# Performance work log

Hardware: AMD Instinct MI355X
Metric: run time of the kernel (lower is better)

Reference implementation:

```python
import jax, jax.numpy as jnp
import numpy as np

N = 96            # max_nodes == R (all nodes real)
IN_DIM, HID, ZD = 64, 256, 64
E = 1024
U = N * (N - 1) // 2
NUM_LOGITS = U + N   # 4656
MPM_ITERS = 50
BN_EPS = 1e-5

def _xavier_relu(k, fi, fo):
    # xavier_uniform with gain('relu') = sqrt(2)
    s = (2.0 ** 0.5) * (6.0 / (fi + fo)) ** 0.5
    return jax.random.uniform(k, (fi, fo), jnp.float32, -s, s)

def setup_inputs() -> dict:
    key = jax.random.key(0)
    ks = jax.random.split(key, 12)
    x = jax.random.normal(ks[0], (N, IN_DIM), jnp.float32)
    edge_index = jnp.stack([jax.random.randint(ks[1], (E,), 0, N),
                            jax.random.randint(ks[2], (E,), 0, N)]).astype(jnp.int32)
    a = (jax.random.uniform(ks[3], (N, N)) < 0.06).astype(jnp.float32)
    adj_gt = jnp.maximum(a, a.T) * (1.0 - jnp.eye(N, dtype=jnp.float32))
    return dict(
        x=x, edge_index=edge_index, adj_gt=adj_gt,
        W1=_xavier_relu(ks[4], IN_DIM, HID), b1=jnp.zeros(HID, jnp.float32),
        gamma1=jnp.ones(HID, jnp.float32), beta1=jnp.zeros(HID, jnp.float32),
        W2=_xavier_relu(ks[5], HID, HID), b2=jnp.zeros(HID, jnp.float32),
        gamma2=jnp.ones(HID, jnp.float32), beta2=jnp.zeros(HID, jnp.float32),
        Wmu=_xavier_relu(ks[6], HID, ZD), bmu=jnp.zeros(ZD, jnp.float32),
        Wlv=_xavier_relu(ks[7], HID, ZD), blv=jnp.zeros(ZD, jnp.float32),
        Wd1=_xavier_relu(ks[8], ZD, HID), bd1=jnp.zeros(HID, jnp.float32),
        Wd2=_xavier_relu(ks[9], HID, NUM_LOGITS), bd2=jnp.zeros(NUM_LOGITS, jnp.float32),
        eps=jax.random.normal(ks[10], (ZD,), jnp.float32))

def _bn(h, g, b):
    # BatchNorm1d, training mode: normalize over nodes (axis 0)
    m = h.mean(0)
    v = h.var(0)
    return (h - m) * jax.lax.rsqrt(v + BN_EPS) * g + b

def _forward(x, adj_gt, W1, b1, gamma1, beta1, W2, b2, gamma2, beta2,
             Wmu, bmu, Wlv, blv, Wd1, bd1, Wd2, bd2, eps, edge_index):
    ar = jnp.arange(N)
    eye = jnp.eye(N, dtype=bool)
    A = jnp.zeros((N, N), jnp.float32).at[edge_index[0], edge_index[1]].set(1.0)
    A = jnp.maximum(A, jnp.eye(N, dtype=jnp.float32))  # self loops
    dinv = jax.lax.rsqrt(A.sum(1))
    A_norm = A * dinv[:, None] * dinv[None, :]
    h = jax.nn.relu(_bn(A_norm @ (x @ W1) + b1, gamma1, beta1))
    h = jax.nn.relu(_bn(A_norm @ (h @ W2) + b2, gamma2, beta2))
    # ---- readout, reparam, decode ----
    g_vec = h.sum(0) / N                      # divide by real node count R
    mu = g_vec @ Wmu + bmu
    lv = jnp.clip(g_vec @ Wlv + blv, -4.0, 4.0)
    z = mu + eps * jnp.exp(0.5 * lv)
    vec = jnp.tanh(jax.nn.relu(z @ Wd1 + bd1) @ Wd2 + bd2)  # [NUM_LOGITS]
    # ---- vec_to_adj ----
    iu = jnp.triu_indices(N, 1)
    Ah = jnp.zeros((N, N), jnp.float32).at[iu].set(vec[:U])
    Ah = (Ah + Ah.T).at[ar, ar].set(vec[U:])  # adjacency logits
    # ---- edge similarity tensor S[i,j,a,b] ----
    Agt = adj_gt.at[ar, ar].set(1.0)
    B = jax.nn.sigmoid(Ah).at[ar, ar].set(1.0)
    degA, degB = Agt.sum(1), B.sum(1)
    node_sim = 1.0 / (jnp.abs(degA[:, None] - degB[None, :]) + 1.0)  # [N,N]
    dA, dB = jnp.diag(Agt), jnp.diag(B)
    S = (Agt[:, :, None, None] * dA[:, None, None, None] * dA[None, :, None, None]
         * B[None, None, :, :] * dB[None, None, :, None] * dB[None, None, None, :])
    xor = eye[:, :, None, None] ^ eye[None, None, :, :]
    S = jnp.where(xor, 0.0, S)
    diag_val = dA[:, None] * dB[None, :] * node_sim  # value at (i,i,a,a)
    both = eye[:, :, None, None] & eye[None, None, :, :]
    S = jnp.where(both, diag_val[:, None, :, None], S)
    # ---- MPM iteration (fixed 50 steps) ----
    nd = S[ar[:, None], ar[:, None], ar[None, :], ar[None, :]]  # node sim [N,N]
    offmask = (~eye)[:, :, None].astype(S.dtype)                # [N,N,1] over (i,j)
    def step(X, _):
        node_term = X * nd
        XS_max = (S * X[None, :, None, :]).max(-1)  # (i,j,a): max_b X[j,b]*S[i,j,a,b]
        edge_term = (XS_max * offmask).sum(1)       # sum over j != i
        Xn = node_term + edge_term
        Xn = Xn / jnp.linalg.norm(Xn)               # Frobenius norm
        return Xn, None
    X0 = jnp.full((N, N), 1.0 / N, jnp.float32)
    X, _ = jax.lax.scan(jax.checkpoint(step), X0, None, length=MPM_ITERS)
    return X

def reference(x, edge_index, adj_gt, W1, b1, gamma1, beta1, W2, b2, gamma2, beta2,
              Wmu, bmu, Wlv, blv, Wd1, bd1, Wd2, bd2, eps):
    return _forward(x, adj_gt, W1, b1, gamma1, beta1, W2, b2, gamma2, beta2,
                    Wmu, bmu, Wlv, blv, Wd1, bd1, Wd2, bd2, eps, edge_index)
```

## Files before the change

kernel.cpp:

```cpp
#include <hip/hip_runtime.h>
#include <math.h>

#define NN    96
#define EE    1024
#define HID   256
#define IND   64
#define ZD    64
#define NL    4656
#define NBLK  96
#define NTHR  384
#define ITERS 50
#define NBARS 57
#define SHF   (HID*49)

struct Params {
  const float* x; const int* ei; const float* adj;
  const float* W1; const float* b1; const float* g1; const float* be1;
  const float* W2; const float* b2; const float* g2; const float* be2;
  const float* Wmu; const float* bmu; const float* Wlv; const float* blv;
  const float* Wd1; const float* bd1; const float* Wd2; const float* bd2;
  const float* eps; float* out;
};

__device__ float d_XW[NN*HID];
__device__ float d_H1pre[NN*HID];
__device__ float d_HW2[NN*HID];
__device__ float d_H2pre[NN*HID];
__device__ float d_mean1[HID], d_istd1[HID];
__device__ float d_gvec[HID];
__device__ float d_vec[NL];
__device__ float d_Xg[2][NN*NN];
__device__ float d_ssq[ITERS+1];
__device__ int   d_flag[NBLK];
__device__ int   d_epoch;

__device__ __forceinline__ float gld(const float* p) {
  return __hip_atomic_load(p, __ATOMIC_RELAXED, __HIP_MEMORY_SCOPE_AGENT);
}
__device__ __forceinline__ void gst(float* p, float v) {
  __hip_atomic_store(p, v, __ATOMIC_RELAXED, __HIP_MEMORY_SCOPE_AGENT);
}

__device__ __forceinline__ float wsum(float v) {
  v += __shfl_xor(v, 32, 64);
  v += __shfl_xor(v, 16, 64);
  v += __shfl_xor(v,  8, 64);
  v += __shfl_xor(v,  4, 64);
  v += __shfl_xor(v,  2, 64);
  v += __shfl_xor(v,  1, 64);
  return v;
}

__device__ __forceinline__ int tri_idx(int a, int c) {
  return a*95 - (a*(a-1))/2 + (c - a - 1);
}

__device__ __forceinline__ void gbar(int idx, int base) {
  asm volatile("s_waitcnt vmcnt(0)" ::: "memory");
  __syncthreads();
  const int tgt = base + idx + 1;
  if (threadIdx.x == 0)
    __hip_atomic_store(&d_flag[blockIdx.x], tgt, __ATOMIC_RELAXED, __HIP_MEMORY_SCOPE_AGENT);
  if (threadIdx.x < NBLK) {
    while (__hip_atomic_load(&d_flag[threadIdx.x], __ATOMIC_RELAXED, __HIP_MEMORY_SCOPE_AGENT) < tgt)
      __builtin_amdgcn_s_sleep(2);
  }
  __syncthreads();
}

__global__ void __launch_bounds__(NTHR) gvae_kernel(Params p) {
  const int b = blockIdx.x;
  const int t = threadIdx.x;

  __shared__ __align__(16) float SH[SHF];
  __shared__ float pre1[HID];
  __shared__ float sg[HID], sd1[HID], sz[ZD];
  __shared__ float dinv[NN];
  __shared__ float eV[NN];   __shared__ int eL[NN];  __shared__ int s_ecnt;
  __shared__ float ndrow[NN], rowsq[NN];    __shared__ int nbrL[NN];
  __shared__ float sdegA;    __shared__ int s_cnt;

  const int base = __hip_atomic_load(&d_epoch, __ATOMIC_RELAXED, __HIP_MEMORY_SCOPE_AGENT) * NBARS;

  for (int i = t; i < NN*97; i += NTHR) SH[i] = 0.0f;
  __syncthreads();
  for (int e = t; e < EE; e += NTHR) {
    int s = p.ei[e], d = p.ei[EE + e];
    SH[s*97 + d] = 1.0f;
  }
  if (t < NN) SH[t*97 + t] = 1.0f;
  __syncthreads();
  if (t < NN) {
    float s = 0.0f;
    for (int j = 0; j < NN; ++j) s += SH[t*97 + j];
    dinv[t] = 1.0f / sqrtf(s);
  }
  if (t < 64) {
    bool is1 = SH[b*97 + t] > 0.5f;
    unsigned long long m1 = __ballot(is1);
    if (is1) eL[__popcll(m1 & ((1ull << t) - 1))] = t;
    int c1 = __popcll(m1);
    bool is2 = (t < 32) && SH[b*97 + 64 + t] > 0.5f;
    unsigned long long m2 = __ballot(is2);
    if (is2) eL[c1 + __popcll(m2 & ((1ull << t) - 1))] = 64 + t;
    if (t == 0) s_ecnt = c1 + __popcll(m2);
  }
  __syncthreads();
  if (t < s_ecnt) eV[t] = dinv[b] * dinv[eL[t]];
  if (t < HID) {
    float acc = 0.0f;
    for (int d = 0; d < IND; ++d) acc += p.x[b*IND + d] * p.W1[d*HID + t];
    gst(&d_XW[b*HID + t], acc);
  }
  if (t < NN) gst(&d_Xg[0][b*NN + t], 1.0f/96.0f);
  if (b == 0 && t <= ITERS) gst(&d_ssq[t], (t == 0) ? 1.0f : 0.0f);
  gbar(0, base);

  {
    const int lim = s_ecnt * HID;
    float tv[16];
    #pragma unroll
    for (int r = 0; r < 16; ++r) {
      int idx = t + r*NTHR;
      if (idx < lim) tv[r] = gld(&d_XW[eL[idx >> 8]*HID + (idx & 255)]);
    }
    #pragma unroll
    for (int r = 0; r < 16; ++r) {
      int idx = t + r*NTHR;
      if (idx < lim) SH[idx] = tv[r];
    }
    for (int idx = t + 16*NTHR; idx < lim; idx += NTHR)
      SH[idx] = gld(&d_XW[eL[idx >> 8]*HID + (idx & 255)]);
    __syncthreads();
    if (t < HID) {
      float acc = 0.0f;
      const int ec = s_ecnt;
      for (int n = 0; n < ec; ++n) acc += eV[n] * SH[n*HID + t];
      acc += p.b1[t];
      pre1[t] = acc;
      gst(&d_H1pre[b*HID + t], acc);
    }
  }
  gbar(1, base);

  if (b < 86) {
    int w = t >> 6, lane = t & 63;
    int c = b*3 + w;
    if (w < 3 && c < HID) {
      float v0 = gld(&d_H1pre[lane*HID + c]);
      float v1 = (lane < 32) ? gld(&d_H1pre[(64+lane)*HID + c]) : 0.0f;
      float mean = wsum(v0 + v1) * (1.0f/96.0f);
      float a0 = v0 - mean, a1 = (lane < 32) ? (v1 - mean) : 0.0f;
      float var = wsum(a0*a0 + a1*a1) * (1.0f/96.0f);
      if (lane == 0) { gst(&d_mean1[c], mean); gst(&d_istd1[c], 1.0f/sqrtf(var + 1e-5f)); }
    }
  }
  gbar(2, base);

  if (t < HID) {
    float m = gld(&d_mean1[t]), is = gld(&d_istd1[t]);
    pre1[t] = fmaxf((pre1[t] - m) * is * p.g1[t] + p.be1[t], 0.0f);
  }
  __syncthreads();
  if (t < HID) {
    float acc = 0.0f;
    for (int k = 0; k < HID; ++k) acc += pre1[k] * p.W2[k*HID + t];
    gst(&d_HW2[b*HID + t], acc);
  }
  gbar(3, base);

  {
    const int lim = s_ecnt * HID;
    float tv[16];
    #pragma unroll
    for (int r = 0; r < 16; ++r) {
      int idx = t + r*NTHR;
      if (idx < lim) tv[r] = gld(&d_HW2[eL[idx >> 8]*HID + (idx & 255)]);
    }
    #pragma unroll
    for (int r = 0; r < 16; ++r) {
      int idx = t + r*NTHR;
      if (idx < lim) SH[idx] = tv[r];
    }
    for (int idx = t + 16*NTHR; idx < lim; idx += NTHR)
      SH[idx] = gld(&d_HW2[eL[idx >> 8]*HID + (idx & 255)]);
    __syncthreads();
    if (t < HID) {
      float acc = 0.0f;
      const int ec = s_ecnt;
      for (int n = 0; n < ec; ++n) acc += eV[n] * SH[n*HID + t];
      acc += p.b2[t];
      gst(&d_H2pre[b*HID + t], acc);
    }
  }
  gbar(4, base);

  if (b < 86) {
    int w = t >> 6, lane = t & 63;
    int c = b*3 + w;
    if (w < 3 && c < HID) {
      float v0 = gld(&d_H2pre[lane*HID + c]);
      float v1 = (lane < 32) ? gld(&d_H2pre[(64+lane)*HID + c]) : 0.0f;
      float mean = wsum(v0 + v1) * (1.0f/96.0f);
      float a0 = v0 - mean, a1 = (lane < 32) ? (v1 - mean) : 0.0f;
      float var = wsum(a0*a0 + a1*a1) * (1.0f/96.0f);
      float is = 1.0f / sqrtf(var + 1e-5f);
      float ga = p.g2[c], be = p.be2[c];
      float h0 = fmaxf((v0 - mean)*is*ga + be, 0.0f);
      float h1v = (lane < 32) ? fmaxf((v1 - mean)*is*ga + be, 0.0f) : 0.0f;
      float gs = wsum(h0 + h1v);
      if (lane == 0) gst(&d_gvec[c], gs * (1.0f/96.0f));
    }
  }
  gbar(5, base);

  if (t < HID) sg[t] = gld(&d_gvec[t]);
  __syncthreads();
  if (t < ZD) {
    float am = p.bmu[t], al = p.blv[t];
    for (int c = 0; c < HID; ++c) {
      float gv = sg[c];
      am += gv * p.Wmu[c*ZD + t];
      al += gv * p.Wlv[c*ZD + t];
    }
    al = fminf(fmaxf(al, -4.0f), 4.0f);
    sz[t] = am + p.eps[t] * expf(0.5f * al);
  }
  __syncthreads();
  if (t < HID) {
    float acc = p.bd1[t];
    for (int d = 0; d < ZD; ++d) acc += sz[d] * p.Wd1[d*HID + t];
    sd1[t] = fmaxf(acc, 0.0f);
  }
  __syncthreads();
  {
    const int o0 = b*49;
    const int nout = min(49, NL - o0);
    #pragma unroll 4
    for (int idx = t; idx < HID*49; idx += NTHR) {
      int k = idx / 49, o = idx - k*49;
      SH[idx] = (o0 + o < NL) ? p.Wd2[k*NL + o0 + o] : 0.0f;
    }
    __syncthreads();
    if (t < nout) {
      float acc = p.bd2[o0 + t];
      for (int k = 0; k < HID; ++k) acc += sd1[k] * SH[k*49 + t];
      gst(&d_vec[o0 + t], tanhf(acc));
    }
  }
  gbar(6, base);

  {
    float tv[13];
    #pragma unroll
    for (int r = 0; r < 13; ++r) {
      int idx = t + r*NTHR;
      if (idx < NL) tv[r] = gld(&d_vec[idx]);
    }
    #pragma unroll
    for (int r = 0; r < 13; ++r) {
      int idx = t + r*NTHR;
      if (idx < NL) SH[idx] = tv[r];
    }
  }
  const int kk = t >> 2;
  const int qq = t & 3;
  if (t < 64) {
    float s = p.adj[b*NN + t] + ((t < 32) ? p.adj[b*NN + 64 + t] : 0.0f);
    s = wsum(s);
    if (t == 0) sdegA = s + 1.0f;
    bool is1 = (t != b) && (p.adj[b*NN + t] > 0.5f);
    unsigned long long m1 = __ballot(is1);
    if (is1) nbrL[__popcll(m1 & ((1ull << t) - 1))] = t;
    int c1 = __popcll(m1);
    bool is2 = (t < 32) && ((64 + t) != b) && (p.adj[b*NN + 64 + t] > 0.5f);
    unsigned long long m2 = __ballot(is2);
    if (is2) nbrL[c1 + __popcll(m2 & ((1ull << t) - 1))] = 64 + t;
    if (t == 0) s_cnt = c1 + __popcll(m2);
  }
  __syncthreads();

  float breg[24];
  {
    float bs = 0.0f;
    const int lb = qq*24;
    #pragma unroll
    for (int s = 0; s < 24; ++s) {
      int l = lb + s;
      float v = 0.0f;
      if (l != kk) {
        int a  = kk < l ? kk : l;
        int cc = kk < l ? l : kk;
        v = 1.0f / (1.0f + expf(-SH[tri_idx(a, cc)]));
      }
      breg[s] = v;
      bs += v;
    }
    float tot = bs + __shfl_xor(bs, 1, 64);
    tot += __shfl_xor(tot, 2, 64);
    if (qq == 0) ndrow[kk] = 1.0f / (fabsf(sdegA - (tot + 1.0f)) + 1.0f);
  }
  __syncthreads();

  int cur = 0;
  for (int it = 0; it < ITERS; ++it) {
    float s2 = gld(&d_ssq[it]);
    int ex;
    (void)frexpf(sqrtf(s2), &ex);
    float scale = ldexpf(1.0f, -ex);
    const int cnt = s_cnt;
    const int lim = (cnt + 1) * NN;
    const float* Xs = d_Xg[cur];
    {
      float tv[8];
      #pragma unroll
      for (int r = 0; r < 8; ++r) {
        int idx = t + r*NTHR;
        if (idx < lim) {
          int slot = idx / NN, col = idx - slot*NN;
          int j = (slot == cnt) ? b : nbrL[slot];
          tv[r] = gld(&Xs[j*NN + col]);
        }
      }
      #pragma unroll
      for (int r = 0; r < 8; ++r) {
        int idx = t + r*NTHR;
        if (idx < lim) SH[idx] = tv[r] * scale;
      }
      for (int idx = t + 8*NTHR; idx < lim; idx += NTHR) {
        int slot = idx / NN, col = idx - slot*NN;
        int j = (slot == cnt) ? b : nbrL[slot];
        SH[idx] = gld(&Xs[j*NN + col]) * scale;
      }
    }
    __syncthreads();

    float acc = 0.0f;
    for (int n = 0; n < cnt; ++n) {
      const float4* xp = reinterpret_cast<const float4*>(&SH[n*NN + qq*24]);
      float vm = 0.0f;
      #pragma unroll
      for (int s6 = 0; s6 < 6; ++s6) {
        float4 xv = xp[s6];
        vm = fmaxf(vm, breg[4*s6+0] * xv.x);
        vm = fmaxf(vm, breg[4*s6+1] * xv.y);
        vm = fmaxf(vm, breg[4*s6+2] * xv.z);
        vm = fmaxf(vm, breg[4*s6+3] * xv.w);
      }
      vm = fmaxf(vm, __shfl_xor(vm, 1, 64));
      vm = fmaxf(vm, __shfl_xor(vm, 2, 64));
      acc += vm;
    }
    if (qq == 0) {
      float xn = SH[cnt*NN + kk] * ndrow[kk] + acc;
      gst(&d_Xg[cur ^ 1][b*NN + kk], xn);
      rowsq[kk] = xn * xn;
    }
    __syncthreads();
    if (t < 64) {
      float v = rowsq[t] + ((t < 32) ? rowsq[64 + t] : 0.0f);
      v = wsum(v);
      if (t == 0)
        __hip_atomic_fetch_add(&d_ssq[it+1], v, __ATOMIC_RELAXED, __HIP_MEMORY_SCOPE_AGENT);
    }
    gbar(7 + it, base);
    cur ^= 1;
  }

  if (t < NN) {
    float inv = 1.0f / sqrtf(gld(&d_ssq[ITERS]));
    p.out[b*NN + t] = gld(&d_Xg[cur][b*NN + t]) * inv;
  }
  if (b == 0 && t == 0)
    __hip_atomic_fetch_add(&d_epoch, 1, __ATOMIC_RELAXED, __HIP_MEMORY_SCOPE_AGENT);
}

extern "C" void kernel_launch(void* const* d_in, const int* in_sizes, int n_in,
                              void* d_out, int out_size, void* d_ws, size_t ws_size,
                              hipStream_t stream) {
  Params prm;
  prm.x   = (const float*)d_in[0];
  prm.ei  = (const int*  )d_in[1];
  prm.adj = (const float*)d_in[2];
  prm.W1  = (const float*)d_in[3];
  prm.b1  = (const float*)d_in[4];
  prm.g1  = (const float*)d_in[5];
  prm.be1 = (const float*)d_in[6];
  prm.W2  = (const float*)d_in[7];
  prm.b2  = (const float*)d_in[8];
  prm.g2  = (const float*)d_in[9];
  prm.be2 = (const float*)d_in[10];
  prm.Wmu = (const float*)d_in[11];
  prm.bmu = (const float*)d_in[12];
  prm.Wlv = (const float*)d_in[13];
  prm.blv = (const float*)d_in[14];
  prm.Wd1 = (const float*)d_in[15];
  prm.bd1 = (const float*)d_in[16];
  prm.Wd2 = (const float*)d_in[17];
  prm.bd2 = (const float*)d_in[18];
  prm.eps = (const float*)d_in[19];
  prm.out = (float*)d_out;

  void* args[] = { &prm };
  hipLaunchCooperativeKernel(reinterpret_cast<void*>(&gvae_kernel),
                             dim3(NBLK), dim3(NTHR), args, 0, stream);
}
```

Before: 525.9 us.

## Fuse two MPM iterations per grid barrier using precomputed max terms

Restructures the 50-step MPM loop into 25 double-steps, each separated by one grid-wide barrier instead of two. Each block exchanges both X and a precomputed per-row max term M through global memory. It then computes the intermediate iterate for its neighbour rows locally from full-graph adjacency lists built in shared memory. This halves the number of global barriers, which dominate the iterative phase, at the cost of redundant per-block computation, larger per-step global reads (the full M matrix) and extra shared-memory use. Normalisation is applied with a power-of-two scale once per double-step, relying on the scale-invariance of the normalized iteration.

```diff
diff --git a/kernel.cpp b/kernel.cpp
--- a/kernel.cpp
+++ b/kernel.cpp
@@ -1,17 +1,20 @@
 #include <hip/hip_runtime.h>
 #include <math.h>
 
-#define NN    96
-#define EE    1024
-#define HID   256
-#define IND   64
-#define ZD    64
-#define NL    4656
-#define NBLK  96
-#define NTHR  384
-#define ITERS 50
-#define NBARS 57
-#define SHF   (HID*49)
+#define NN     96
+#define EE     1024
+#define HID    256
+#define IND    64
+#define ZD     64
+#define NL     4656
+#define NBLK   96
+#define NTHR   384
+#define ITERS  50
+#define DSTEPS 25
+#define NBARS  33
+#define SHF    12544
+#define XOFF   9216
+#define LISTCAP 1536
 
 struct Params {
   const float* x; const int* ei; const float* adj;
@@ -30,7 +33,8 @@
 __device__ float d_gvec[HID];
 __device__ float d_vec[NL];
 __device__ float d_Xg[2][NN*NN];
-__device__ float d_ssq[ITERS+1];
+__device__ float d_M[2][NN*NN];
+__device__ float d_ssq[DSTEPS+1];
 __device__ int   d_flag[NBLK];
 __device__ int   d_epoch;
 
@@ -77,8 +81,11 @@
   __shared__ float sg[HID], sd1[HID], sz[ZD];
   __shared__ float dinv[NN];
   __shared__ float eV[NN];   __shared__ int eL[NN];  __shared__ int s_ecnt;
-  __shared__ float ndrow[NN], rowsq[NN];    __shared__ int nbrL[NN];
-  __shared__ float sdegA;    __shared__ int s_cnt;
+  __shared__ float rowsq[NN], xb2[NN], sdegB[NN];
+  __shared__ int   scnt[NN];
+  __shared__ int   s_off[NN+1];
+  __shared__ int   s_list[LISTCAP];
+  __shared__ unsigned long long smask[NN][2];
 
   const int base = __hip_atomic_load(&d_epoch, __ATOMIC_RELAXED, __HIP_MEMORY_SCOPE_AGENT) * NBARS;
 
@@ -113,7 +120,7 @@
     gst(&d_XW[b*HID + t], acc);
   }
   if (t < NN) gst(&d_Xg[0][b*NN + t], 1.0f/96.0f);
-  if (b == 0 && t <= ITERS) gst(&d_ssq[t], (t == 0) ? 1.0f : 0.0f);
+  if (b == 0 && t <= DSTEPS) gst(&d_ssq[t], (t == 0) ? 1.0f : 0.0f);
   gbar(0, base);
 
   {
@@ -263,23 +270,42 @@
       if (idx < NL) SH[idx] = tv[r];
     }
   }
+  {
+    const int w = t >> 6, lane = t & 63;
+    #pragma unroll
+    for (int i = 0; i < 16; ++i) {
+      const int j = w*16 + i;
+      float a1 = p.adj[j*NN + lane];
+      float a2 = (lane < 32) ? p.adj[j*NN + 64 + lane] : 0.0f;
+      unsigned long long m1 = __ballot(a1 > 0.5f);
+      unsigned long long m2 = __ballot((lane < 32) && (a2 > 0.5f));
+      if (lane == 0) {
+        smask[j][0] = m1; smask[j][1] = m2;
+        scnt[j] = __popcll(m1) + __popcll(m2);
+      }
+    }
+  }
+  __syncthreads();
+  if (t == 0) {
+    int acc = 0;
+    for (int j = 0; j < NN; ++j) { s_off[j] = acc; acc += scnt[j]; }
+    s_off[NN] = acc;
+  }
+  __syncthreads();
+  {
+    const int w = t >> 6, lane = t & 63;
+    #pragma unroll
+    for (int i = 0; i < 16; ++i) {
+      const int j = w*16 + i;
+      unsigned long long m1 = smask[j][0], m2 = smask[j][1];
+      if ((m1 >> lane) & 1)
+        s_list[s_off[j] + __popcll(m1 & ((1ull << lane) - 1))] = lane;
+      if (lane < 32 && ((m2 >> lane) & 1))
+        s_list[s_off[j] + __popcll(m1) + __popcll(m2 & ((1ull << lane) - 1))] = 64 + lane;
+    }
+  }
   const int kk = t >> 2;
   const int qq = t & 3;
-  if (t < 64) {
-    float s = p.adj[b*NN + t] + ((t < 32) ? p.adj[b*NN + 64 + t] : 0.0f);
-    s = wsum(s);
-    if (t == 0) sdegA = s + 1.0f;
-    bool is1 = (t != b) && (p.adj[b*NN + t] > 0.5f);
-    unsigned long long m1 = __ballot(is1);
-    if (is1) nbrL[__popcll(m1 & ((1ull << t) - 1))] = t;
-    int c1 = __popcll(m1);
-    bool is2 = (t < 32) && ((64 + t) != b) && (p.adj[b*NN + 64 + t] > 0.5f);
-    unsigned long long m2 = __ballot(is2);
-    if (is2) nbrL[c1 + __popcll(m2 & ((1ull << t) - 1))] = 64 + t;
-    if (t == 0) s_cnt = c1 + __popcll(m2);
-  }
-  __syncthreads();
-
   float breg[24];
   {
     float bs = 0.0f;
@@ -298,46 +324,70 @@
     }
     float tot = bs + __shfl_xor(bs, 1, 64);
     tot += __shfl_xor(tot, 2, 64);
-    if (qq == 0) ndrow[kk] = 1.0f / (fabsf(sdegA - (tot + 1.0f)) + 1.0f);
-  }
-  __syncthreads();
-
+    if (qq == 0) sdegB[kk] = tot + 1.0f;
+  }
+  {
+    float vm = 0.0f;
+    #pragma unroll
+    for (int s = 0; s < 24; ++s) vm = fmaxf(vm, breg[s] * (1.0f/96.0f));
+    vm = fmaxf(vm, __shfl_xor(vm, 1, 64));
+    vm = fmaxf(vm, __shfl_xor(vm, 2, 64));
+    if (qq == 0) gst(&d_M[0][b*NN + kk], vm);
+  }
+  gbar(7, base);
+
+  const int  myoff = s_off[b];
+  const int  cnt   = s_off[b+1] - myoff;
+  const float dAb  = (float)(scnt[b] + 1);
   int cur = 0;
-  for (int it = 0; it < ITERS; ++it) {
-    float s2 = gld(&d_ssq[it]);
+  for (int ds = 0; ds < DSTEPS; ++ds) {
+    float s2 = gld(&d_ssq[ds]);
     int ex;
     (void)frexpf(sqrtf(s2), &ex);
-    float scale = ldexpf(1.0f, -ex);
-    const int cnt = s_cnt;
-    const int lim = (cnt + 1) * NN;
+    const float scale = ldexpf(1.0f, -ex);
+    const float* Ms = d_M[cur];
     const float* Xs = d_Xg[cur];
+    const int limX = (cnt + 1) * NN;
     {
-      float tv[8];
+      float tm[24], tx[8];
+      #pragma unroll
+      for (int r = 0; r < 24; ++r) tm[r] = gld(&Ms[t + r*NTHR]);
       #pragma unroll
       for (int r = 0; r < 8; ++r) {
         int idx = t + r*NTHR;
-        if (idx < lim) {
+        if (idx < limX) {
           int slot = idx / NN, col = idx - slot*NN;
-          int j = (slot == cnt) ? b : nbrL[slot];
-          tv[r] = gld(&Xs[j*NN + col]);
+          int j = (slot == cnt) ? b : s_list[myoff + slot];
+          tx[r] = gld(&Xs[j*NN + col]);
         }
       }
+      #pragma unroll
+      for (int r = 0; r < 24; ++r) SH[t + r*NTHR] = tm[r] * scale;
       #pragma unroll
       for (int r = 0; r < 8; ++r) {
         int idx = t + r*NTHR;
-        if (idx < lim) SH[idx] = tv[r] * scale;
-      }
-      for (int idx = t + 8*NTHR; idx < lim; idx += NTHR) {
+        if (idx < limX) SH[XOFF + idx] = tx[r] * scale;
+      }
+      for (int idx = t + 8*NTHR; idx < limX; idx += NTHR) {
         int slot = idx / NN, col = idx - slot*NN;
-        int j = (slot == cnt) ? b : nbrL[slot];
-        SH[idx] = gld(&Xs[j*NN + col]) * scale;
-      }
-    }
-    __syncthreads();
-
-    float acc = 0.0f;
-    for (int n = 0; n < cnt; ++n) {
-      const float4* xp = reinterpret_cast<const float4*>(&SH[n*NN + qq*24]);
+        int j = (slot == cnt) ? b : s_list[myoff + slot];
+        SH[XOFF + idx] = gld(&Xs[j*NN + col]) * scale;
+      }
+    }
+    __syncthreads();
+    for (int idx = t; idx < limX; idx += NTHR) {
+      int slot = idx / NN, k = idx - slot*NN;
+      int j = (slot == cnt) ? b : s_list[myoff + slot];
+      float dAj = (float)(scnt[j] + 1);
+      float es = 0.0f;
+      const int o1 = s_off[j+1];
+      for (int ptr = s_off[j]; ptr < o1; ++ptr)
+        es += SH[s_list[ptr]*NN + k];
+      SH[XOFF + idx] = SH[XOFF + idx] * (1.0f / (fabsf(dAj - sdegB[k]) + 1.0f)) + es;
+    }
+    __syncthreads();
+    for (int s = 0; s < cnt; ++s) {
+      const float4* xp = reinterpret_cast<const float4*>(&SH[XOFF + s*NN + qq*24]);
       float vm = 0.0f;
       #pragma unroll
       for (int s6 = 0; s6 < 6; ++s6) {
@@ -349,27 +399,40 @@
       }
       vm = fmaxf(vm, __shfl_xor(vm, 1, 64));
       vm = fmaxf(vm, __shfl_xor(vm, 2, 64));
-      acc += vm;
-    }
+      if (qq == 0) SH[s*NN + kk] = vm;
+    }
+    __syncthreads();
     if (qq == 0) {
-      float xn = SH[cnt*NN + kk] * ndrow[kk] + acc;
+      float es = 0.0f;
+      for (int s = 0; s < cnt; ++s) es += SH[s*NN + kk];
+      float xn = SH[XOFF + cnt*NN + kk] * (1.0f / (fabsf(dAb - sdegB[kk]) + 1.0f)) + es;
+      xb2[kk] = xn;
+      rowsq[kk] = xn * xn;
       gst(&d_Xg[cur ^ 1][b*NN + kk], xn);
-      rowsq[kk] = xn * xn;
-    }
-    __syncthreads();
+    }
+    __syncthreads();
+    {
+      const int lb = qq*24;
+      float vm = 0.0f;
+      #pragma unroll
+      for (int s = 0; s < 24; ++s) vm = fmaxf(vm, breg[s] * xb2[lb + s]);
+      vm = fmaxf(vm, __shfl_xor(vm, 1, 64));
+      vm = fmaxf(vm, __shfl_xor(vm, 2, 64));
+      if (qq == 0) gst(&d_M[cur ^ 1][b*NN + kk], vm);
+    }
     if (t < 64) {
       float v = rowsq[t] + ((t < 32) ? rowsq[64 + t] : 0.0f);
       v = wsum(v);
       if (t == 0)
-        __hip_atomic_fetch_add(&d_ssq[it+1], v, __ATOMIC_RELAXED, __HIP_MEMORY_SCOPE_AGENT);
-    }
-    gbar(7 + it, base);
+        __hip_atomic_fetch_add(&d_ssq[ds+1], v, __ATOMIC_RELAXED, __HIP_MEMORY_SCOPE_AGENT);
+    }
+    gbar(8 + ds, base);
     cur ^= 1;
   }
 
   if (t < NN) {
-    float inv = 1.0f / sqrtf(gld(&d_ssq[ITERS]));
-    p.out[b*NN + t] = gld(&d_Xg[cur][b*NN + t]) * inv;
+    float inv = 1.0f / sqrtf(gld(&d_ssq[DSTEPS]));
+    p.out[b*NN + t] = xb2[t] * inv;
   }
   if (b == 0 && t == 0)
     __hip_atomic_fetch_add(&d_epoch, 1, __ATOMIC_RELAXED, __HIP_MEMORY_SCOPE_AGENT);
```

After: 568.1 us. +8.0%, slower.

## Use master-release grid barrier and per-block partial norms instead of atomics

Applied to the files above, without the earlier changes.

Replaces the all-to-all flag-polling grid barrier with a centralized one: block 0 polls all flags and then publishes a single release word, which the other blocks wait on with one thread. The global atomic fetch-add of the squared norm is replaced by per-block partial sums in a double-buffered array, which each block reduces locally after the barrier. The norm scaling is applied to the new X after the matvec rather than to the loaded tile, and the final output uses a shared copy of the block's row. This cuts atomic contention and polling traffic, at the cost of an extra hop through block 0 per barrier and a small local reduction each iteration.

```diff
diff --git a/kernel.cpp b/kernel.cpp
--- a/kernel.cpp
+++ b/kernel.cpp
@@ -30,8 +30,9 @@
 __device__ float d_gvec[HID];
 __device__ float d_vec[NL];
 __device__ float d_Xg[2][NN*NN];
-__device__ float d_ssq[ITERS+1];
+__device__ float d_part[2][NN];
 __device__ int   d_flag[NBLK];
+__device__ int   d_rel;
 __device__ int   d_epoch;
 
 __device__ __forceinline__ float gld(const float* p) {
@@ -59,13 +60,23 @@
   asm volatile("s_waitcnt vmcnt(0)" ::: "memory");
   __syncthreads();
   const int tgt = base + idx + 1;
-  if (threadIdx.x == 0)
-    __hip_atomic_store(&d_flag[blockIdx.x], tgt, __ATOMIC_RELAXED, __HIP_MEMORY_SCOPE_AGENT);
-  if (threadIdx.x < NBLK) {
-    while (__hip_atomic_load(&d_flag[threadIdx.x], __ATOMIC_RELAXED, __HIP_MEMORY_SCOPE_AGENT) < tgt)
-      __builtin_amdgcn_s_sleep(2);
-  }
-  __syncthreads();
+  const int t = threadIdx.x;
+  if (blockIdx.x == 0) {
+    if (t >= 1 && t < NBLK) {
+      while (__hip_atomic_load(&d_flag[t], __ATOMIC_RELAXED, __HIP_MEMORY_SCOPE_AGENT) < tgt)
+        __builtin_amdgcn_s_sleep(1);
+    }
+    __syncthreads();
+    if (t == 0)
+      __hip_atomic_store(&d_rel, tgt, __ATOMIC_RELAXED, __HIP_MEMORY_SCOPE_AGENT);
+  } else {
+    if (t == 0) {
+      __hip_atomic_store(&d_flag[blockIdx.x], tgt, __ATOMIC_RELAXED, __HIP_MEMORY_SCOPE_AGENT);
+      while (__hip_atomic_load(&d_rel, __ATOMIC_RELAXED, __HIP_MEMORY_SCOPE_AGENT) < tgt)
+        __builtin_amdgcn_s_sleep(1);
+    }
+    __syncthreads();
+  }
 }
 
 __global__ void __launch_bounds__(NTHR) gvae_kernel(Params p) {
@@ -77,8 +88,10 @@
   __shared__ float sg[HID], sd1[HID], sz[ZD];
   __shared__ float dinv[NN];
   __shared__ float eV[NN];   __shared__ int eL[NN];  __shared__ int s_ecnt;
-  __shared__ float ndrow[NN], rowsq[NN];    __shared__ int nbrL[NN];
+  __shared__ float ndrow[NN], rowsq[NN], xb2[NN];
+  __shared__ int   nbrL[NN];
   __shared__ float sdegA;    __shared__ int s_cnt;
+  __shared__ float sF;
 
   const int base = __hip_atomic_load(&d_epoch, __ATOMIC_RELAXED, __HIP_MEMORY_SCOPE_AGENT) * NBARS;
 
@@ -113,7 +126,6 @@
     gst(&d_XW[b*HID + t], acc);
   }
   if (t < NN) gst(&d_Xg[0][b*NN + t], 1.0f/96.0f);
-  if (b == 0 && t <= ITERS) gst(&d_ssq[t], (t == 0) ? 1.0f : 0.0f);
   gbar(0, base);
 
   {
@@ -304,34 +316,45 @@
 
   int cur = 0;
   for (int it = 0; it < ITERS; ++it) {
-    float s2 = gld(&d_ssq[it]);
-    int ex;
-    (void)frexpf(sqrtf(s2), &ex);
-    float scale = ldexpf(1.0f, -ex);
     const int cnt = s_cnt;
     const int lim = (cnt + 1) * NN;
     const float* Xs = d_Xg[cur];
-    {
-      float tv[8];
-      #pragma unroll
-      for (int r = 0; r < 8; ++r) {
-        int idx = t + r*NTHR;
-        if (idx < lim) {
-          int slot = idx / NN, col = idx - slot*NN;
-          int j = (slot == cnt) ? b : nbrL[slot];
-          tv[r] = gld(&Xs[j*NN + col]);
-        }
-      }
-      #pragma unroll
-      for (int r = 0; r < 8; ++r) {
-        int idx = t + r*NTHR;
-        if (idx < lim) SH[idx] = tv[r] * scale;
-      }
-      for (int idx = t + 8*NTHR; idx < lim; idx += NTHR) {
+    float pj = 0.0f;
+    if (it > 0 && t < NN) pj = gld(&d_part[(it-1) & 1][t]);
+    float tv[8];
+    #pragma unroll
+    for (int r = 0; r < 8; ++r) {
+      int idx = t + r*NTHR;
+      if (idx < lim) {
         int slot = idx / NN, col = idx - slot*NN;
         int j = (slot == cnt) ? b : nbrL[slot];
-        SH[idx] = gld(&Xs[j*NN + col]) * scale;
+        tv[r] = gld(&Xs[j*NN + col]);
       }
+    }
+    float s2 = 1.0f;
+    if (it > 0) {
+      if (t < NN) rowsq[t] = pj;
+      __syncthreads();
+      if (t < 64) {
+        float v = rowsq[t] + ((t < 32) ? rowsq[64 + t] : 0.0f);
+        v = wsum(v);
+        if (t == 0) sF = v;
+      }
+      __syncthreads();
+      s2 = sF;
+    }
+    int ex;
+    (void)frexpf(sqrtf(s2), &ex);
+    const float scale = ldexpf(1.0f, -ex);
+    #pragma unroll
+    for (int r = 0; r < 8; ++r) {
+      int idx = t + r*NTHR;
+      if (idx < lim) SH[idx] = tv[r];
+    }
+    for (int idx = t + 8*NTHR; idx < lim; idx += NTHR) {
+      int slot = idx / NN, col = idx - slot*NN;
+      int j = (slot == cnt) ? b : nbrL[slot];
+      SH[idx] = gld(&Xs[j*NN + col]);
     }
     __syncthreads();
 
@@ -352,25 +375,31 @@
       acc += vm;
     }
     if (qq == 0) {
-      float xn = SH[cnt*NN + kk] * ndrow[kk] + acc;
+      float xn = scale * (SH[cnt*NN + kk] * ndrow[kk] + acc);
+      xb2[kk] = xn;
+      rowsq[kk] = xn * xn;
       gst(&d_Xg[cur ^ 1][b*NN + kk], xn);
-      rowsq[kk] = xn * xn;
     }
     __syncthreads();
     if (t < 64) {
       float v = rowsq[t] + ((t < 32) ? rowsq[64 + t] : 0.0f);
       v = wsum(v);
-      if (t == 0)
-        __hip_atomic_fetch_add(&d_ssq[it+1], v, __ATOMIC_RELAXED, __HIP_MEMORY_SCOPE_AGENT);
+      if (t == 0) gst(&d_part[it & 1][b], v);
     }
     gbar(7 + it, base);
     cur ^= 1;
   }
 
-  if (t < NN) {
-    float inv = 1.0f / sqrtf(gld(&d_ssq[ITERS]));
-    p.out[b*NN + t] = gld(&d_Xg[cur][b*NN + t]) * inv;
-  }
+  if (t < NN) rowsq[t] = gld(&d_part[(ITERS-1) & 1][t]);
+  __syncthreads();
+  if (t < 64) {
+    float v = rowsq[t] + ((t < 32) ? rowsq[64 + t] : 0.0f);
+    v = wsum(v);
+    if (t == 0) sF = v;
+  }
+  __syncthreads();
+  if (t < NN) p.out[b*NN + t] = xb2[t] * (1.0f / sqrtf(sF));
+
   if (b == 0 && t == 0)
     __hip_atomic_fetch_add(&d_epoch, 1, __ATOMIC_RELAXED, __HIP_MEMORY_SCOPE_AGENT);
 }
```

Measured after the change: 535.6 us. No clear change (+1.8%).
